# Kernel tuning notes

Hardware: AMD Instinct MI355X
Metric: run time of the kernel (lower is better)

## Reference

```python
import jax, jax.numpy as jnp
import numpy as np


def _log_kernel(ks, sigma):
    ax = np.arange(-(ks // 2), ks // 2 + 1, dtype=np.float64)
    xx, yy = np.meshgrid(ax, ax, indexing='ij')
    r2 = xx ** 2 + yy ** 2
    gaussian = np.exp(-r2 / (2 * sigma ** 2))
    laplacian = -1.0 / (np.pi * sigma ** 4) * (1.0 - r2 / (2 * sigma ** 2))
    k = laplacian * gaussian
    k = k / np.sum(np.abs(k))
    return jnp.asarray(k, jnp.float32)


def _hpf_kernel(ks):
    if ks == 3:
        k = np.array([[-1, -1, -1], [-1, 8, -1], [-1, -1, -1]], dtype=np.float32)
    else:  # 5
        k = -np.ones((5, 5), dtype=np.float32)
        k[2, 2] = 24.0
    return jnp.asarray(k)


def _lpf_kernel():
    k = np.array([[1, 2, 1], [2, 4, 2], [1, 2, 1]], dtype=np.float32) / 16.0
    return jnp.asarray(k)


def _gabor_kernel(angle, frequency=0.1, sigma_x=2.0, sigma_y=2.0):
    theta = np.radians(angle)
    x, y = np.meshgrid(np.linspace(-3, 3, 7), np.linspace(-3, 3, 7))
    x_t = x * np.cos(theta) + y * np.sin(theta)
    y_t = -x * np.sin(theta) + y * np.cos(theta)
    g = np.exp(-(x_t ** 2 / sigma_x ** 2 + y_t ** 2 / sigma_y ** 2) / 2.0) * np.cos(2 * np.pi * frequency * x_t)
    g = g / np.sum(np.abs(g))
    return jnp.asarray(g, jnp.float32)


def _dwconv(x, k2d, pad):
    # depthwise conv: same single-channel kernel applied to every channel
    C = x.shape[1]
    kern = jnp.broadcast_to(k2d[None, None], (C, 1) + k2d.shape)  # (C,1,kh,kw)
    return jax.lax.conv_general_dilated(
        x, kern, window_strides=(1, 1), padding=[(pad, pad), (pad, pad)],
        feature_group_count=C, dimension_numbers=('NCHW', 'OIHW', 'NCHW'))


def _squash(z):
    # (tanh(z*0.1)+1)/2
    return (jnp.tanh(z * 0.1) + 1.0) * 0.5


def setup_inputs() -> dict:
    key = jax.random.key(0)
    x = jax.random.normal(key, (16, 3, 512, 512), dtype=jnp.float32)
    return {"x": x, "use_gabor": 1}


def reference(x, use_gabor):
    # 'original'
    original = x
    # 'lpf'
    lpf = _dwconv(x, _lpf_kernel(), pad=1)
    # 'log': multi-scale LoG -> squash -> elementwise max over scales
    log3 = _dwconv(x, _log_kernel(3, 0.8), pad=1)
    log5 = _dwconv(x, _log_kernel(5, 1.0), pad=2)
    log7 = _dwconv(x, _log_kernel(7, 1.4), pad=3)
    log_out = jnp.maximum(jnp.maximum(_squash(log3), _squash(log5)), _squash(log7))
    # 'hpf'
    hpf3 = _dwconv(x, _hpf_kernel(3), pad=1)
    hpf5 = _dwconv(x, _hpf_kernel(5), pad=2)
    hpf_out = jnp.maximum(_squash(hpf3), _squash(hpf5))
    outs = (original, lpf, log_out, hpf_out)
    if use_gabor:
        gab = None
        for angle in (0, 45, 90, 135):
            r = jnp.tanh(_dwconv(x, _gabor_kernel(angle), pad=3) * 0.1)
            gab = r if gab is None else jnp.maximum(gab, r)
        outs = outs + (gab,)
    return outs
```

## Files before the change

### kernel.cpp

```cpp
#include <hip/hip_runtime.h>

#define IMG_H 512
#define IMG_W 512
#define TILE_W 64
#define TILE_H 16
#define LDSW 72
#define LDSH 22
#define NTHREADS 256


constexpr double PI_D = 3.141592653589793238462643383279502884;

constexpr double cexp(double x) {
  double term = 1.0, sum = 1.0;
  for (int n = 1; n < 48; ++n) { term *= x / n; sum += term; }
  return sum;
}
constexpr double ccos(double x) {
  double term = 1.0, sum = 1.0;
  for (int n = 1; n < 24; ++n) {
    term *= -x * x / ((2.0 * n - 1.0) * (2.0 * n));
    sum += term;
  }
  return sum;
}
constexpr double csin(double x) {
  double term = x, sum = x;
  for (int n = 1; n < 24; ++n) {
    term *= -x * x / ((2.0 * n) * (2.0 * n + 1.0));
    sum += term;
  }
  return sum;
}
constexpr double cabs_(double x) { return x < 0 ? -x : x; }

struct KTabs {
  float lpf[9];
  float log3[9];
  float log5[25];
  float log7[49];
  float hpf3[9];
  float hpf5[25];
  float gab[4][49];
};

constexpr void fill_log(int ks, double sigma, float* out) {
  double buf[49] = {};
  double s = 0.0;
  const int h = ks / 2;
  for (int i = 0; i < ks; ++i) {
    for (int j = 0; j < ks; ++j) {
      const double xi = (double)(i - h);
      const double yj = (double)(j - h);
      const double r2 = xi * xi + yj * yj;
      const double g = cexp(-r2 / (2.0 * sigma * sigma));
      const double lap = -1.0 / (PI_D * sigma * sigma * sigma * sigma) *
                         (1.0 - r2 / (2.0 * sigma * sigma));
      buf[i * ks + j] = lap * g;
      s += cabs_(lap * g);
    }
  }
  for (int k = 0; k < ks * ks; ++k) out[k] = (float)(buf[k] / s);
}

constexpr void fill_gabor(double ang_deg, float* out) {
  const double th = ang_deg * PI_D / 180.0;
  const double ct = ccos(th), st = csin(th);
  double buf[49] = {};
  double s = 0.0;
  for (int i = 0; i < 7; ++i) {
    for (int j = 0; j < 7; ++j) {
      const double xv = (double)(j - 3);
      const double yv = (double)(i - 3);
      const double xt = xv * ct + yv * st;
      const double yt = -xv * st + yv * ct;
      const double g = cexp(-(xt * xt / 4.0 + yt * yt / 4.0) / 2.0) *
                       ccos(2.0 * PI_D * 0.1 * xt);
      buf[i * 7 + j] = g;
      s += cabs_(g);
    }
  }
  for (int k = 0; k < 49; ++k) out[k] = (float)(buf[k] / s);
}

constexpr KTabs make_tabs() {
  KTabs t{};
  const double lv[9] = {1, 2, 1, 2, 4, 2, 1, 2, 1};
  for (int k = 0; k < 9; ++k) t.lpf[k] = (float)(lv[k] / 16.0);
  for (int k = 0; k < 9; ++k) t.hpf3[k] = -1.0f;
  t.hpf3[4] = 8.0f;
  for (int k = 0; k < 25; ++k) t.hpf5[k] = -1.0f;
  t.hpf5[12] = 24.0f;
  fill_log(3, 0.8, t.log3);
  fill_log(5, 1.0, t.log5);
  fill_log(7, 1.4, t.log7);
  fill_gabor(0.0, t.gab[0]);
  fill_gabor(45.0, t.gab[1]);
  fill_gabor(90.0, t.gab[2]);
  fill_gabor(135.0, t.gab[3]);
  return t;
}

constexpr KTabs KT = make_tabs();


__device__ __forceinline__ float fast_tanh(float x) {
  float e = __builtin_amdgcn_exp2f(x * 2.8853900817779268f);
  return 1.0f - 2.0f * __builtin_amdgcn_rcpf(e + 1.0f);
}
__device__ __forceinline__ float squash_from(float z) {
  return fmaf(fast_tanh(0.1f * z), 0.5f, 0.5f);
}

__global__ __launch_bounds__(NTHREADS)
void msif_kernel(const float* __restrict__ x, float* __restrict__ out,
                 int planes, int do_gab) {
  __shared__ float tile[LDSH * LDSW];
  const int tid = threadIdx.x;
  const int tx = tid & 15;
  const int ty = tid >> 4;
  const int x0 = blockIdx.x * TILE_W;
  const int y0 = blockIdx.y * TILE_H;
  const int plane = blockIdx.z;
  const float* __restrict__ in = x + (size_t)plane * (IMG_H * IMG_W);

  const int gx0 = x0 - 4;
  const int gy0 = y0 - 3;
  for (int k = tid; k < LDSH * (LDSW / 4); k += NTHREADS) {
    int r = k / (LDSW / 4);
    int cc = (k - r * (LDSW / 4)) * 4;
    int gy = gy0 + r;
    int gx = gx0 + cc;
    float4 v = make_float4(0.f, 0.f, 0.f, 0.f);
    if ((unsigned)gy < IMG_H) {
      const float* rowp = in + (size_t)gy * IMG_W;
      if (gx >= 0 && gx + 3 < IMG_W) {
        v = *(const float4*)(rowp + gx);
      } else {
        float t0 = 0.f, t1 = 0.f, t2 = 0.f, t3 = 0.f;
        if ((unsigned)(gx + 0) < IMG_W) t0 = rowp[gx + 0];
        if ((unsigned)(gx + 1) < IMG_W) t1 = rowp[gx + 1];
        if ((unsigned)(gx + 2) < IMG_W) t2 = rowp[gx + 2];
        if ((unsigned)(gx + 3) < IMG_W) t3 = rowp[gx + 3];
        v = make_float4(t0, t1, t2, t3);
      }
    }
    *(float4*)&tile[r * LDSW + cc] = v;
  }
  __syncthreads();

  float l7[4] = {}, l5[4] = {}, l3[4] = {};
  float h5[4] = {}, h3[4] = {}, lp[4] = {};
  float g0[4] = {}, g1[4] = {}, g2[4] = {}, g3[4] = {};

#pragma unroll
  for (int ir = 0; ir < 7; ++ir) {
    const float4* p = (const float4*)&tile[(ty + ir) * LDSW + 4 * tx];
    float4 w0 = p[0], w1 = p[1], w2 = p[2];
    float w[12] = {w0.x, w0.y, w0.z, w0.w, w1.x, w1.y, w1.z, w1.w,
                   w2.x, w2.y, w2.z, w2.w};

#pragma unroll
    for (int dx = 0; dx < 7; ++dx) {
      const float c7 = KT.log7[ir * 7 + dx];
      const float cg0 = KT.gab[0][ir * 7 + dx];
      const float cg1 = KT.gab[1][ir * 7 + dx];
      const float cg2 = KT.gab[2][ir * 7 + dx];
      const float cg3 = KT.gab[3][ir * 7 + dx];
#pragma unroll
      for (int c = 0; c < 4; ++c) {
        const float v = w[c + dx + 1];
        l7[c] = fmaf(v, c7, l7[c]);
        g0[c] = fmaf(v, cg0, g0[c]);
        g1[c] = fmaf(v, cg1, g1[c]);
        g2[c] = fmaf(v, cg2, g2[c]);
        g3[c] = fmaf(v, cg3, g3[c]);
      }
    }
    if (ir >= 1 && ir <= 5) {
      const int kr = ir - 1;
#pragma unroll
      for (int dx = 0; dx < 5; ++dx) {
        const float c5 = KT.log5[kr * 5 + dx];
        const float ch5 = KT.hpf5[kr * 5 + dx];
#pragma unroll
        for (int c = 0; c < 4; ++c) {
          const float v = w[c + dx + 2];
          l5[c] = fmaf(v, c5, l5[c]);
          h5[c] = fmaf(v, ch5, h5[c]);
        }
      }
    }
    if (ir >= 2 && ir <= 4) {
      const int kr = ir - 2;
#pragma unroll
      for (int dx = 0; dx < 3; ++dx) {
        const float cl = KT.lpf[kr * 3 + dx];
        const float c3 = KT.log3[kr * 3 + dx];
        const float ch3 = KT.hpf3[kr * 3 + dx];
#pragma unroll
        for (int c = 0; c < 4; ++c) {
          const float v = w[c + dx + 3];
          lp[c] = fmaf(v, cl, lp[c]);
          l3[c] = fmaf(v, c3, l3[c]);
          h3[c] = fmaf(v, ch3, h3[c]);
        }
      }
    }
  }

  const int X = x0 + 4 * tx;
  const int yo = y0 + ty;
  const size_t fs = (size_t)planes * (IMG_H * IMG_W);
  const size_t off = (size_t)plane * (IMG_H * IMG_W) + (size_t)yo * IMG_W + X;

  float4 orig = *(const float4*)&tile[(ty + 3) * LDSW + 4 * tx + 4];
  *(float4*)(out + off) = orig;

  float lo[4], ho[4], go[4];
#pragma unroll
  for (int c = 0; c < 4; ++c) {
    lo[c] = squash_from(fmaxf(fmaxf(l3[c], l5[c]), l7[c]));
    ho[c] = squash_from(fmaxf(h3[c], h5[c]));
    go[c] = fast_tanh(0.1f * fmaxf(fmaxf(g0[c], g1[c]), fmaxf(g2[c], g3[c])));
  }
  *(float4*)(out + fs + off) = make_float4(lp[0], lp[1], lp[2], lp[3]);
  *(float4*)(out + 2 * fs + off) = make_float4(lo[0], lo[1], lo[2], lo[3]);
  *(float4*)(out + 3 * fs + off) = make_float4(ho[0], ho[1], ho[2], ho[3]);
  if (do_gab)
    *(float4*)(out + 4 * fs + off) = make_float4(go[0], go[1], go[2], go[3]);
}

extern "C" void kernel_launch(void* const* d_in, const int* in_sizes, int n_in,
                              void* d_out, int out_size, void* d_ws, size_t ws_size,
                              hipStream_t stream) {
  const float* x = (const float*)d_in[0];
  float* out = (float*)d_out;
  const int plane_elems = IMG_H * IMG_W;
  const int planes = in_sizes[0] / plane_elems;
  const int do_gab = (out_size >= 5 * in_sizes[0]) ? 1 : 0;

  dim3 grid(IMG_W / TILE_W, IMG_H / TILE_H, planes);
  msif_kernel<<<grid, NTHREADS, 0, stream>>>(x, out, planes, do_gab);
}
```

Baseline: 317.3 us.

## Decompose LoG, Gabor and HPF stencils into separable vertical/horizontal passes via LDS

```diff
diff --git a/kernel.cpp b/kernel.cpp
--- a/kernel.cpp
+++ b/kernel.cpp
@@ -6,6 +6,8 @@
 #define TILE_H 16
 #define LDSW 72
 #define LDSH 22
+#define TCOLS 72
+#define TROWS 16
 #define NTHREADS 256
 
 
@@ -33,16 +35,6 @@
   return sum;
 }
 constexpr double cabs_(double x) { return x < 0 ? -x : x; }
-
-struct KTabs {
-  float lpf[9];
-  float log3[9];
-  float log5[25];
-  float log7[49];
-  float hpf3[9];
-  float hpf5[25];
-  float gab[4][49];
-};
 
 constexpr void fill_log(int ks, double sigma, float* out) {
   double buf[49] = {};
@@ -63,12 +55,33 @@
   for (int k = 0; k < ks * ks; ++k) out[k] = (float)(buf[k] / s);
 }
 
-constexpr void fill_gabor(double ang_deg, float* out) {
+constexpr void fill_log_sep(int ks, double sigma, float* va, float* g, float* wb) {
+  const int h = ks / 2;
+  double s = 0.0;
+  for (int i = 0; i < ks; ++i)
+    for (int j = 0; j < ks; ++j) {
+      const double xi = (double)(i - h), yj = (double)(j - h);
+      const double r2 = xi * xi + yj * yj;
+      const double gg = cexp(-r2 / (2.0 * sigma * sigma));
+      const double lap = -1.0 / (PI_D * sigma * sigma * sigma * sigma) *
+                         (1.0 - r2 / (2.0 * sigma * sigma));
+      s += cabs_(lap * gg);
+    }
+  const double c = 1.0 / (PI_D * sigma * sigma * sigma * sigma);
+  for (int i = 0; i < ks; ++i) {
+    const double d = (double)(i - h);
+    const double gi = cexp(-d * d / (2.0 * sigma * sigma));
+    g[i] = (float)gi;
+    va[i] = (float)((-c + c * d * d / (2.0 * sigma * sigma)) * gi / s);
+    wb[i] = (float)((c * d * d / (2.0 * sigma * sigma)) * gi / s);
+  }
+}
+
+constexpr double gabor_norm(double ang_deg) {
   const double th = ang_deg * PI_D / 180.0;
   const double ct = ccos(th), st = csin(th);
-  double buf[49] = {};
   double s = 0.0;
-  for (int i = 0; i < 7; ++i) {
+  for (int i = 0; i < 7; ++i)
     for (int j = 0; j < 7; ++j) {
       const double xv = (double)(j - 3);
       const double yv = (double)(i - 3);
@@ -76,32 +89,51 @@
       const double yt = -xv * st + yv * ct;
       const double g = cexp(-(xt * xt / 4.0 + yt * yt / 4.0) / 2.0) *
                        ccos(2.0 * PI_D * 0.1 * xt);
-      buf[i * 7 + j] = g;
       s += cabs_(g);
     }
-  }
-  for (int k = 0; k < 49; ++k) out[k] = (float)(buf[k] / s);
-}
-
-constexpr KTabs make_tabs() {
-  KTabs t{};
-  const double lv[9] = {1, 2, 1, 2, 4, 2, 1, 2, 1};
-  for (int k = 0; k < 9; ++k) t.lpf[k] = (float)(lv[k] / 16.0);
-  for (int k = 0; k < 9; ++k) t.hpf3[k] = -1.0f;
-  t.hpf3[4] = 8.0f;
-  for (int k = 0; k < 25; ++k) t.hpf5[k] = -1.0f;
-  t.hpf5[12] = 24.0f;
-  fill_log(3, 0.8, t.log3);
-  fill_log(5, 1.0, t.log5);
-  fill_log(7, 1.4, t.log7);
-  fill_gabor(0.0, t.gab[0]);
-  fill_gabor(45.0, t.gab[1]);
-  fill_gabor(90.0, t.gab[2]);
-  fill_gabor(135.0, t.gab[3]);
+  return s;
+}
+
+struct SepTabs {
+  float l5_va[5], l5_g[5], l5_wb[5];
+  float l7_va[7], l7_g[7], l7_wb[7];
+  float v_gb[7], v_gc0[7], v_gca[7], v_gsa[7];
+  float h_g0[7], h_g90[7], h_gc[7], h_gs[7];
+  float is45, is135;
+  float l3_m, l3_e, l3_s;
+};
+
+constexpr SepTabs make_sep() {
+  SepTabs t{};
+  fill_log_sep(5, 1.0, t.l5_va, t.l5_g, t.l5_wb);
+  fill_log_sep(7, 1.4, t.l7_va, t.l7_g, t.l7_wb);
+  const double s0 = gabor_norm(0.0), s90 = gabor_norm(90.0);
+  const double s45 = gabor_norm(45.0), s135 = gabor_norm(135.0);
+  const double th45 = 45.0 * PI_D / 180.0;
+  const double a45 = 2.0 * PI_D * 0.1 * ccos(th45);
+  const double b45 = 2.0 * PI_D * 0.1 * csin(th45);
+  const double w0 = 2.0 * PI_D * 0.1;
+  for (int k = 0; k < 7; ++k) {
+    const double d = (double)(k - 3);
+    const double gg = cexp(-d * d / 8.0);
+    t.v_gb[k]  = (float)gg;
+    t.v_gc0[k] = (float)(gg * ccos(w0 * d));
+    t.v_gca[k] = (float)(gg * ccos(b45 * d));
+    t.v_gsa[k] = (float)(gg * csin(b45 * d));
+    t.h_g0[k]  = (float)(gg * ccos(w0 * d) / s0);
+    t.h_g90[k] = (float)(gg / s90);
+    t.h_gc[k]  = (float)(gg * ccos(a45 * d));
+    t.h_gs[k]  = (float)(gg * csin(a45 * d));
+  }
+  t.is45 = (float)(1.0 / s45);
+  t.is135 = (float)(1.0 / s135);
+  float l3[9] = {};
+  fill_log(3, 0.8, l3);
+  t.l3_m = l3[4]; t.l3_e = l3[1]; t.l3_s = l3[0];
   return t;
 }
 
-constexpr KTabs KT = make_tabs();
+constexpr SepTabs ST = make_sep();
 
 
 __device__ __forceinline__ float fast_tanh(float x) {
@@ -111,11 +143,39 @@
 __device__ __forceinline__ float squash_from(float z) {
   return fmaf(fast_tanh(0.1f * z), 0.5f, 0.5f);
 }
+__device__ __forceinline__ float4 f4z() { return make_float4(0.f, 0.f, 0.f, 0.f); }
+__device__ __forceinline__ float4 f4add(float4 a, float4 b) {
+  return make_float4(a.x + b.x, a.y + b.y, a.z + b.z, a.w + b.w);
+}
+__device__ __forceinline__ float4 f4fma(float a, float4 b, float4 c) {
+  return make_float4(fmaf(a, b.x, c.x), fmaf(a, b.y, c.y),
+                     fmaf(a, b.z, c.z), fmaf(a, b.w, c.w));
+}
+__device__ __forceinline__ void loadw12(const float* p, float* w) {
+  const float4 a = *(const float4*)(p);
+  const float4 b = *(const float4*)(p + 4);
+  const float4 c = *(const float4*)(p + 8);
+  w[0] = a.x; w[1] = a.y; w[2] = a.z; w[3] = a.w;
+  w[4] = b.x; w[5] = b.y; w[6] = b.z; w[7] = b.w;
+  w[8] = c.x; w[9] = c.y; w[10] = c.z; w[11] = c.w;
+}
+
+#define T_B5  0
+#define T_L5A 1
+#define T_L5G 2
+#define T_L7A 3
+#define T_L7G 4
+#define T_GB  5
+#define T_GC0 6
+#define T_GCA 7
+#define T_GSA 8
 
 __global__ __launch_bounds__(NTHREADS)
 void msif_kernel(const float* __restrict__ x, float* __restrict__ out,
                  int planes, int do_gab) {
   __shared__ float tile[LDSH * LDSW];
+  __shared__ float T[9][TROWS * TCOLS];
+
   const int tid = threadIdx.x;
   const int tx = tid & 15;
   const int ty = tid >> 4;
@@ -149,80 +209,137 @@
   }
   __syncthreads();
 
-  float l7[4] = {}, l5[4] = {}, l3[4] = {};
-  float h5[4] = {}, h3[4] = {}, lp[4] = {};
-  float g0[4] = {}, g1[4] = {}, g2[4] = {}, g3[4] = {};
-
-#pragma unroll
-  for (int ir = 0; ir < 7; ++ir) {
-    const float4* p = (const float4*)&tile[(ty + ir) * LDSW + 4 * tx];
-    float4 w0 = p[0], w1 = p[1], w2 = p[2];
-    float w[12] = {w0.x, w0.y, w0.z, w0.w, w1.x, w1.y, w1.z, w1.w,
-                   w2.x, w2.y, w2.z, w2.w};
-
-#pragma unroll
-    for (int dx = 0; dx < 7; ++dx) {
-      const float c7 = KT.log7[ir * 7 + dx];
-      const float cg0 = KT.gab[0][ir * 7 + dx];
-      const float cg1 = KT.gab[1][ir * 7 + dx];
-      const float cg2 = KT.gab[2][ir * 7 + dx];
-      const float cg3 = KT.gab[3][ir * 7 + dx];
-#pragma unroll
-      for (int c = 0; c < 4; ++c) {
-        const float v = w[c + dx + 1];
-        l7[c] = fmaf(v, c7, l7[c]);
-        g0[c] = fmaf(v, cg0, g0[c]);
-        g1[c] = fmaf(v, cg1, g1[c]);
-        g2[c] = fmaf(v, cg2, g2[c]);
-        g3[c] = fmaf(v, cg3, g3[c]);
-      }
-    }
-    if (ir >= 1 && ir <= 5) {
-      const int kr = ir - 1;
-#pragma unroll
-      for (int dx = 0; dx < 5; ++dx) {
-        const float c5 = KT.log5[kr * 5 + dx];
-        const float ch5 = KT.hpf5[kr * 5 + dx];
-#pragma unroll
-        for (int c = 0; c < 4; ++c) {
-          const float v = w[c + dx + 2];
-          l5[c] = fmaf(v, c5, l5[c]);
-          h5[c] = fmaf(v, ch5, h5[c]);
-        }
-      }
-    }
-    if (ir >= 2 && ir <= 4) {
-      const int kr = ir - 2;
-#pragma unroll
-      for (int dx = 0; dx < 3; ++dx) {
-        const float cl = KT.lpf[kr * 3 + dx];
-        const float c3 = KT.log3[kr * 3 + dx];
-        const float ch3 = KT.hpf3[kr * 3 + dx];
-#pragma unroll
-        for (int c = 0; c < 4; ++c) {
-          const float v = w[c + dx + 3];
-          lp[c] = fmaf(v, cl, lp[c]);
-          l3[c] = fmaf(v, c3, l3[c]);
-          h3[c] = fmaf(v, ch3, h3[c]);
-        }
-      }
-    }
-  }
+  for (int k = tid; k < TROWS * (TCOLS / 4); k += NTHREADS) {
+    const int r = k / (TCOLS / 4);
+    const int c4 = (k - r * (TCOLS / 4)) * 4;
+    const float* base = &tile[r * LDSW + c4];
+    float4 wv[7];
+#pragma unroll
+    for (int i = 0; i < 7; ++i) wv[i] = *(const float4*)(base + i * LDSW);
+
+    float4 b5 = f4add(f4add(wv[1], wv[2]), f4add(f4add(wv[3], wv[4]), wv[5]));
+    float4 l5a = f4z(), l5g = f4z();
+#pragma unroll
+    for (int i = 0; i < 5; ++i) {
+      l5a = f4fma(ST.l5_va[i], wv[i + 1], l5a);
+      l5g = f4fma(ST.l5_g[i],  wv[i + 1], l5g);
+    }
+    float4 l7a = f4z(), l7g = f4z(), gb = f4z(), gc0 = f4z(), gca = f4z(), gsa = f4z();
+#pragma unroll
+    for (int i = 0; i < 7; ++i) {
+      l7a = f4fma(ST.l7_va[i], wv[i], l7a);
+      l7g = f4fma(ST.l7_g[i],  wv[i], l7g);
+      gb  = f4fma(ST.v_gb[i],  wv[i], gb);
+      gc0 = f4fma(ST.v_gc0[i], wv[i], gc0);
+      gca = f4fma(ST.v_gca[i], wv[i], gca);
+      gsa = f4fma(ST.v_gsa[i], wv[i], gsa);
+    }
+    const int o = r * TCOLS + c4;
+    *(float4*)&T[T_B5][o]  = b5;
+    *(float4*)&T[T_L5A][o] = l5a;
+    *(float4*)&T[T_L5G][o] = l5g;
+    *(float4*)&T[T_L7A][o] = l7a;
+    *(float4*)&T[T_L7G][o] = l7g;
+    *(float4*)&T[T_GB][o]  = gb;
+    *(float4*)&T[T_GC0][o] = gc0;
+    *(float4*)&T[T_GCA][o] = gca;
+    *(float4*)&T[T_GSA][o] = gsa;
+  }
+  __syncthreads();
+
+  const int toff = ty * TCOLS + 4 * tx;
+  float w[12];
+  float l7[4] = {}, l5[4] = {}, g0[4] = {}, g90[4] = {}, Pa[4] = {}, Qa[4] = {};
+  float box[4];
+
+  loadw12(&T[T_L7A][toff], w);
+#pragma unroll
+  for (int dx = 0; dx < 7; ++dx) {
+    const float cc = ST.l7_g[dx];
+#pragma unroll
+    for (int c = 0; c < 4; ++c) l7[c] = fmaf(w[c + dx + 1], cc, l7[c]);
+  }
+  loadw12(&T[T_L7G][toff], w);
+#pragma unroll
+  for (int dx = 0; dx < 7; ++dx) {
+    const float cc = ST.l7_wb[dx];
+#pragma unroll
+    for (int c = 0; c < 4; ++c) l7[c] = fmaf(w[c + dx + 1], cc, l7[c]);
+  }
+  loadw12(&T[T_L5A][toff], w);
+#pragma unroll
+  for (int dx = 0; dx < 5; ++dx) {
+    const float cc = ST.l5_g[dx];
+#pragma unroll
+    for (int c = 0; c < 4; ++c) l5[c] = fmaf(w[c + dx + 2], cc, l5[c]);
+  }
+  loadw12(&T[T_L5G][toff], w);
+#pragma unroll
+  for (int dx = 0; dx < 5; ++dx) {
+    const float cc = ST.l5_wb[dx];
+#pragma unroll
+    for (int c = 0; c < 4; ++c) l5[c] = fmaf(w[c + dx + 2], cc, l5[c]);
+  }
+  loadw12(&T[T_B5][toff], w);
+#pragma unroll
+  for (int c = 0; c < 4; ++c)
+    box[c] = ((w[c + 2] + w[c + 3]) + (w[c + 4] + w[c + 5])) + w[c + 6];
+  loadw12(&T[T_GB][toff], w);
+#pragma unroll
+  for (int dx = 0; dx < 7; ++dx) {
+    const float cc = ST.h_g0[dx];
+#pragma unroll
+    for (int c = 0; c < 4; ++c) g0[c] = fmaf(w[c + dx + 1], cc, g0[c]);
+  }
+  loadw12(&T[T_GC0][toff], w);
+#pragma unroll
+  for (int dx = 0; dx < 7; ++dx) {
+    const float cc = ST.h_g90[dx];
+#pragma unroll
+    for (int c = 0; c < 4; ++c) g90[c] = fmaf(w[c + dx + 1], cc, g90[c]);
+  }
+  loadw12(&T[T_GCA][toff], w);
+#pragma unroll
+  for (int dx = 0; dx < 7; ++dx) {
+    const float cc = ST.h_gc[dx];
+#pragma unroll
+    for (int c = 0; c < 4; ++c) Pa[c] = fmaf(w[c + dx + 1], cc, Pa[c]);
+  }
+  loadw12(&T[T_GSA][toff], w);
+#pragma unroll
+  for (int dx = 0; dx < 7; ++dx) {
+    const float cc = ST.h_gs[dx];
+#pragma unroll
+    for (int c = 0; c < 4; ++c) Qa[c] = fmaf(w[c + dx + 1], cc, Qa[c]);
+  }
+
+  float tr[12], mr[12], br[12];
+  loadw12(&tile[(ty + 2) * LDSW + 4 * tx], tr);
+  loadw12(&tile[(ty + 3) * LDSW + 4 * tx], mr);
+  loadw12(&tile[(ty + 4) * LDSW + 4 * tx], br);
 
   const int X = x0 + 4 * tx;
   const int yo = y0 + ty;
   const size_t fs = (size_t)planes * (IMG_H * IMG_W);
   const size_t off = (size_t)plane * (IMG_H * IMG_W) + (size_t)yo * IMG_W + X;
 
-  float4 orig = *(const float4*)&tile[(ty + 3) * LDSW + 4 * tx + 4];
-  *(float4*)(out + off) = orig;
-
-  float lo[4], ho[4], go[4];
+  *(float4*)(out + off) = make_float4(mr[4], mr[5], mr[6], mr[7]);
+
+  float lp[4], lo[4], ho[4], go[4];
 #pragma unroll
   for (int c = 0; c < 4; ++c) {
-    lo[c] = squash_from(fmaxf(fmaxf(l3[c], l5[c]), l7[c]));
-    ho[c] = squash_from(fmaxf(h3[c], h5[c]));
-    go[c] = fast_tanh(0.1f * fmaxf(fmaxf(g0[c], g1[c]), fmaxf(g2[c], g3[c])));
+    const float mC = mr[c + 4];
+    const float e  = (tr[c + 4] + br[c + 4]) + (mr[c + 3] + mr[c + 5]);
+    const float sC = (tr[c + 3] + tr[c + 5]) + (br[c + 3] + br[c + 5]);
+    lp[c] = fmaf(0.25f, mC, fmaf(0.125f, e, 0.0625f * sC));
+    const float l3v = fmaf(ST.l3_m, mC, fmaf(ST.l3_e, e, ST.l3_s * sC));
+    const float h3v = fmaf(8.f, mC, -(e + sC));
+    const float h5v = fmaf(25.f, mC, -box[c]);
+    lo[c] = squash_from(fmaxf(fmaxf(l3v, l5[c]), l7[c]));
+    ho[c] = squash_from(fmaxf(h3v, h5v));
+    const float o45  = (Pa[c] - Qa[c]) * ST.is45;
+    const float o135 = (Pa[c] + Qa[c]) * ST.is135;
+    go[c] = fast_tanh(0.1f * fmaxf(fmaxf(g0[c], g90[c]), fmaxf(o45, o135)));
   }
   *(float4*)(out + fs + off) = make_float4(lp[0], lp[1], lp[2], lp[3]);
   *(float4*)(out + 2 * fs + off) = make_float4(lo[0], lo[1], lo[2], lo[3]);
```

Result: slower. 328.5 us (+3.5%).

## Process multiple tiles per block with double-buffered LDS prefetch and nontemporal stores

Applied to the files above, without the earlier changes.

```diff
diff --git a/kernel.cpp b/kernel.cpp
--- a/kernel.cpp
+++ b/kernel.cpp
@@ -4,9 +4,14 @@
 #define IMG_W 512
 #define TILE_W 64
 #define TILE_H 16
+#define TILES_X (IMG_W / TILE_W)
+#define TILES_Y (IMG_H / TILE_H)
+#define TILES_PER_PLANE (TILES_X * TILES_Y)
 #define LDSW 72
 #define LDSH 22
+#define NSLOTS (LDSH * (LDSW / 4))
 #define NTHREADS 256
+#define TPB 12
 
 
 constexpr double PI_D = 3.141592653589793238462643383279502884;
@@ -104,6 +109,8 @@
 constexpr KTabs KT = make_tabs();
 
 
+typedef float f4v __attribute__((ext_vector_type(4)));
+
 __device__ __forceinline__ float fast_tanh(float x) {
   float e = __builtin_amdgcn_exp2f(x * 2.8853900817779268f);
   return 1.0f - 2.0f * __builtin_amdgcn_rcpf(e + 1.0f);
@@ -112,123 +119,175 @@
   return fmaf(fast_tanh(0.1f * z), 0.5f, 0.5f);
 }
 
+__device__ __forceinline__ void store_nt(float* p, float a, float b, float c,
+                                         float d) {
+  f4v v = {a, b, c, d};
+  __builtin_nontemporal_store(v, (f4v*)p);
+}
+
+__device__ __forceinline__ float4 guarded_load(const float* __restrict__ in,
+                                               int gy, int gx) {
+  float4 v = make_float4(0.f, 0.f, 0.f, 0.f);
+  if ((unsigned)gy < IMG_H) {
+    const float* rowp = in + (size_t)gy * IMG_W;
+    if (gx >= 0 && gx + 3 < IMG_W) {
+      v = *(const float4*)(rowp + gx);
+    } else {
+      if ((unsigned)(gx + 0) < IMG_W) v.x = rowp[gx + 0];
+      if ((unsigned)(gx + 1) < IMG_W) v.y = rowp[gx + 1];
+      if ((unsigned)(gx + 2) < IMG_W) v.z = rowp[gx + 2];
+      if ((unsigned)(gx + 3) < IMG_W) v.w = rowp[gx + 3];
+    }
+  }
+  return v;
+}
+
+__device__ __forceinline__ void tile_decode(int t, int& x0, int& y0, int& pl) {
+  pl = t >> 8;
+  const int rem = t & 255;
+  y0 = (rem >> 3) * TILE_H;
+  x0 = (rem & 7) * TILE_W;
+}
+
+
 __global__ __launch_bounds__(NTHREADS)
 void msif_kernel(const float* __restrict__ x, float* __restrict__ out,
-                 int planes, int do_gab) {
-  __shared__ float tile[LDSH * LDSW];
+                 int planes, int do_gab, int tiles_total) {
+  __shared__ float lds[2][LDSH * LDSW];
+
   const int tid = threadIdx.x;
   const int tx = tid & 15;
   const int ty = tid >> 4;
-  const int x0 = blockIdx.x * TILE_W;
-  const int y0 = blockIdx.y * TILE_H;
-  const int plane = blockIdx.z;
-  const float* __restrict__ in = x + (size_t)plane * (IMG_H * IMG_W);
-
-  const int gx0 = x0 - 4;
-  const int gy0 = y0 - 3;
-  for (int k = tid; k < LDSH * (LDSW / 4); k += NTHREADS) {
-    int r = k / (LDSW / 4);
-    int cc = (k - r * (LDSW / 4)) * 4;
-    int gy = gy0 + r;
-    int gx = gx0 + cc;
-    float4 v = make_float4(0.f, 0.f, 0.f, 0.f);
-    if ((unsigned)gy < IMG_H) {
-      const float* rowp = in + (size_t)gy * IMG_W;
-      if (gx >= 0 && gx + 3 < IMG_W) {
-        v = *(const float4*)(rowp + gx);
-      } else {
-        float t0 = 0.f, t1 = 0.f, t2 = 0.f, t3 = 0.f;
-        if ((unsigned)(gx + 0) < IMG_W) t0 = rowp[gx + 0];
-        if ((unsigned)(gx + 1) < IMG_W) t1 = rowp[gx + 1];
-        if ((unsigned)(gx + 2) < IMG_W) t2 = rowp[gx + 2];
-        if ((unsigned)(gx + 3) < IMG_W) t3 = rowp[gx + 3];
-        v = make_float4(t0, t1, t2, t3);
-      }
-    }
-    *(float4*)&tile[r * LDSW + cc] = v;
+  const int rA = tid / (LDSW / 4);
+  const int cA = (tid % (LDSW / 4)) * 4;
+  const int slotB = tid + NTHREADS;
+  const bool hasB = slotB < NSLOTS;
+  const int rB = slotB / (LDSW / 4);
+  const int cB = (slotB % (LDSW / 4)) * 4;
+
+  const int t0 = blockIdx.x * TPB;
+  if (t0 >= tiles_total) return;
+
+  const size_t fs = (size_t)planes * (IMG_H * IMG_W);
+
+  {
+    int x0, y0, pl;
+    tile_decode(t0, x0, y0, pl);
+    const float* in = x + (size_t)pl * (IMG_H * IMG_W);
+    const float4 va = guarded_load(in, y0 - 3 + rA, x0 - 4 + cA);
+    float4 vb = make_float4(0.f, 0.f, 0.f, 0.f);
+    if (hasB) vb = guarded_load(in, y0 - 3 + rB, x0 - 4 + cB);
+    *(float4*)&lds[0][rA * LDSW + cA] = va;
+    if (hasB) *(float4*)&lds[0][rB * LDSW + cB] = vb;
   }
   __syncthreads();
 
-  float l7[4] = {}, l5[4] = {}, l3[4] = {};
-  float h5[4] = {}, h3[4] = {}, lp[4] = {};
-  float g0[4] = {}, g1[4] = {}, g2[4] = {}, g3[4] = {};
-
-#pragma unroll
-  for (int ir = 0; ir < 7; ++ir) {
-    const float4* p = (const float4*)&tile[(ty + ir) * LDSW + 4 * tx];
-    float4 w0 = p[0], w1 = p[1], w2 = p[2];
-    float w[12] = {w0.x, w0.y, w0.z, w0.w, w1.x, w1.y, w1.z, w1.w,
-                   w2.x, w2.y, w2.z, w2.w};
-
-#pragma unroll
-    for (int dx = 0; dx < 7; ++dx) {
-      const float c7 = KT.log7[ir * 7 + dx];
-      const float cg0 = KT.gab[0][ir * 7 + dx];
-      const float cg1 = KT.gab[1][ir * 7 + dx];
-      const float cg2 = KT.gab[2][ir * 7 + dx];
-      const float cg3 = KT.gab[3][ir * 7 + dx];
-#pragma unroll
-      for (int c = 0; c < 4; ++c) {
-        const float v = w[c + dx + 1];
-        l7[c] = fmaf(v, c7, l7[c]);
-        g0[c] = fmaf(v, cg0, g0[c]);
-        g1[c] = fmaf(v, cg1, g1[c]);
-        g2[c] = fmaf(v, cg2, g2[c]);
-        g3[c] = fmaf(v, cg3, g3[c]);
-      }
-    }
-    if (ir >= 1 && ir <= 5) {
-      const int kr = ir - 1;
-#pragma unroll
-      for (int dx = 0; dx < 5; ++dx) {
-        const float c5 = KT.log5[kr * 5 + dx];
-        const float ch5 = KT.hpf5[kr * 5 + dx];
+  int cur = 0;
+  for (int i = 0; i < TPB; ++i) {
+    const int t = t0 + i;
+    if (t >= tiles_total) break;
+    int x0, y0, pl;
+    tile_decode(t, x0, y0, pl);
+    const bool havenext = (i + 1 < TPB) && (t + 1 < tiles_total);
+
+    float4 va = make_float4(0.f, 0.f, 0.f, 0.f);
+    float4 vb = make_float4(0.f, 0.f, 0.f, 0.f);
+    if (havenext) {
+      int nx0, ny0, npl;
+      tile_decode(t + 1, nx0, ny0, npl);
+      const float* nin = x + (size_t)npl * (IMG_H * IMG_W);
+      va = guarded_load(nin, ny0 - 3 + rA, nx0 - 4 + cA);
+      if (hasB) vb = guarded_load(nin, ny0 - 3 + rB, nx0 - 4 + cB);
+    }
+
+    const float* __restrict__ tl = lds[cur];
+
+    float l7[4] = {}, l5[4] = {}, l3[4] = {};
+    float h5[4] = {}, h3[4] = {}, lp[4] = {};
+    float g0[4] = {}, g1[4] = {}, g2[4] = {}, g3[4] = {};
+
+#pragma unroll
+    for (int ir = 0; ir < 7; ++ir) {
+      const float4* p = (const float4*)&tl[(ty + ir) * LDSW + 4 * tx];
+      float4 w0 = p[0], w1 = p[1], w2 = p[2];
+      float w[12] = {w0.x, w0.y, w0.z, w0.w, w1.x, w1.y, w1.z, w1.w,
+                     w2.x, w2.y, w2.z, w2.w};
+
+#pragma unroll
+      for (int dx = 0; dx < 7; ++dx) {
+        const float c7 = KT.log7[ir * 7 + dx];
+        const float cg0 = KT.gab[0][ir * 7 + dx];
+        const float cg1 = KT.gab[1][ir * 7 + dx];
+        const float cg2 = KT.gab[2][ir * 7 + dx];
+        const float cg3 = KT.gab[3][ir * 7 + dx];
 #pragma unroll
         for (int c = 0; c < 4; ++c) {
-          const float v = w[c + dx + 2];
-          l5[c] = fmaf(v, c5, l5[c]);
-          h5[c] = fmaf(v, ch5, h5[c]);
+          const float v = w[c + dx + 1];
+          l7[c] = fmaf(v, c7, l7[c]);
+          g0[c] = fmaf(v, cg0, g0[c]);
+          g1[c] = fmaf(v, cg1, g1[c]);
+          g2[c] = fmaf(v, cg2, g2[c]);
+          g3[c] = fmaf(v, cg3, g3[c]);
         }
       }
-    }
-    if (ir >= 2 && ir <= 4) {
-      const int kr = ir - 2;
-#pragma unroll
-      for (int dx = 0; dx < 3; ++dx) {
-        const float cl = KT.lpf[kr * 3 + dx];
-        const float c3 = KT.log3[kr * 3 + dx];
-        const float ch3 = KT.hpf3[kr * 3 + dx];
-#pragma unroll
-        for (int c = 0; c < 4; ++c) {
-          const float v = w[c + dx + 3];
-          lp[c] = fmaf(v, cl, lp[c]);
-          l3[c] = fmaf(v, c3, l3[c]);
-          h3[c] = fmaf(v, ch3, h3[c]);
+      if (ir >= 1 && ir <= 5) {
+        const int kr = ir - 1;
+#pragma unroll
+        for (int dx = 0; dx < 5; ++dx) {
+          const float c5 = KT.log5[kr * 5 + dx];
+          const float ch5 = KT.hpf5[kr * 5 + dx];
+#pragma unroll
+          for (int c = 0; c < 4; ++c) {
+            const float v = w[c + dx + 2];
+            l5[c] = fmaf(v, c5, l5[c]);
+            h5[c] = fmaf(v, ch5, h5[c]);
+          }
         }
       }
-    }
-  }
-
-  const int X = x0 + 4 * tx;
-  const int yo = y0 + ty;
-  const size_t fs = (size_t)planes * (IMG_H * IMG_W);
-  const size_t off = (size_t)plane * (IMG_H * IMG_W) + (size_t)yo * IMG_W + X;
-
-  float4 orig = *(const float4*)&tile[(ty + 3) * LDSW + 4 * tx + 4];
-  *(float4*)(out + off) = orig;
-
-  float lo[4], ho[4], go[4];
-#pragma unroll
-  for (int c = 0; c < 4; ++c) {
-    lo[c] = squash_from(fmaxf(fmaxf(l3[c], l5[c]), l7[c]));
-    ho[c] = squash_from(fmaxf(h3[c], h5[c]));
-    go[c] = fast_tanh(0.1f * fmaxf(fmaxf(g0[c], g1[c]), fmaxf(g2[c], g3[c])));
-  }
-  *(float4*)(out + fs + off) = make_float4(lp[0], lp[1], lp[2], lp[3]);
-  *(float4*)(out + 2 * fs + off) = make_float4(lo[0], lo[1], lo[2], lo[3]);
-  *(float4*)(out + 3 * fs + off) = make_float4(ho[0], ho[1], ho[2], ho[3]);
-  if (do_gab)
-    *(float4*)(out + 4 * fs + off) = make_float4(go[0], go[1], go[2], go[3]);
+      if (ir >= 2 && ir <= 4) {
+        const int kr = ir - 2;
+#pragma unroll
+        for (int dx = 0; dx < 3; ++dx) {
+          const float cl = KT.lpf[kr * 3 + dx];
+          const float c3 = KT.log3[kr * 3 + dx];
+          const float ch3 = KT.hpf3[kr * 3 + dx];
+#pragma unroll
+          for (int c = 0; c < 4; ++c) {
+            const float v = w[c + dx + 3];
+            lp[c] = fmaf(v, cl, lp[c]);
+            l3[c] = fmaf(v, c3, l3[c]);
+            h3[c] = fmaf(v, ch3, h3[c]);
+          }
+        }
+      }
+    }
+
+    const int X = x0 + 4 * tx;
+    const int yo = y0 + ty;
+    const size_t off = (size_t)pl * (IMG_H * IMG_W) + (size_t)yo * IMG_W + X;
+
+    const float4 orig = *(const float4*)&tl[(ty + 3) * LDSW + 4 * tx + 4];
+    store_nt(out + off, orig.x, orig.y, orig.z, orig.w);
+
+    float lo[4], ho[4], go[4];
+#pragma unroll
+    for (int c = 0; c < 4; ++c) {
+      lo[c] = squash_from(fmaxf(fmaxf(l3[c], l5[c]), l7[c]));
+      ho[c] = squash_from(fmaxf(h3[c], h5[c]));
+      go[c] = fast_tanh(0.1f * fmaxf(fmaxf(g0[c], g1[c]), fmaxf(g2[c], g3[c])));
+    }
+    store_nt(out + fs + off, lp[0], lp[1], lp[2], lp[3]);
+    store_nt(out + 2 * fs + off, lo[0], lo[1], lo[2], lo[3]);
+    store_nt(out + 3 * fs + off, ho[0], ho[1], ho[2], ho[3]);
+    if (do_gab) store_nt(out + 4 * fs + off, go[0], go[1], go[2], go[3]);
+
+    if (havenext) {
+      *(float4*)&lds[cur ^ 1][rA * LDSW + cA] = va;
+      if (hasB) *(float4*)&lds[cur ^ 1][rB * LDSW + cB] = vb;
+      __syncthreads();
+      cur ^= 1;
+    }
+  }
 }
 
 extern "C" void kernel_launch(void* const* d_in, const int* in_sizes, int n_in,
@@ -239,7 +298,9 @@
   const int plane_elems = IMG_H * IMG_W;
   const int planes = in_sizes[0] / plane_elems;
   const int do_gab = (out_size >= 5 * in_sizes[0]) ? 1 : 0;
-
-  dim3 grid(IMG_W / TILE_W, IMG_H / TILE_H, planes);
-  msif_kernel<<<grid, NTHREADS, 0, stream>>>(x, out, planes, do_gab);
-}
+  const int tiles_total = planes * TILES_PER_PLANE;
+  const int nblocks = (tiles_total + TPB - 1) / TPB;
+
+  msif_kernel<<<dim3(nblocks), NTHREADS, 0, stream>>>(x, out, planes, do_gab,
+                                                      tiles_total);
+}
```

Result: slower. 345.1 us (+8.7%).

## Tile full-width row bands per block to eliminate horizontal halo reloads

Applied to the files above, without the earlier changes.

```diff
diff --git a/kernel.cpp b/kernel.cpp
--- a/kernel.cpp
+++ b/kernel.cpp
@@ -2,10 +2,11 @@
 
 #define IMG_H 512
 #define IMG_W 512
-#define TILE_W 64
 #define TILE_H 16
-#define LDSW 72
+#define BANDS (IMG_H / TILE_H)
+#define LDSW 520
 #define LDSH 22
+#define ROWSLOTS (LDSW / 4)
 #define NTHREADS 256
 
 
@@ -112,123 +113,126 @@
   return fmaf(fast_tanh(0.1f * z), 0.5f, 0.5f);
 }
 
+
 __global__ __launch_bounds__(NTHREADS)
 void msif_kernel(const float* __restrict__ x, float* __restrict__ out,
                  int planes, int do_gab) {
   __shared__ float tile[LDSH * LDSW];
+
   const int tid = threadIdx.x;
-  const int tx = tid & 15;
-  const int ty = tid >> 4;
-  const int x0 = blockIdx.x * TILE_W;
-  const int y0 = blockIdx.y * TILE_H;
-  const int plane = blockIdx.z;
-  const float* __restrict__ in = x + (size_t)plane * (IMG_H * IMG_W);
-
-  const int gx0 = x0 - 4;
+  const int lane = tid & 63;
+  const int wv = tid >> 6;
+  const int b = blockIdx.x;
+  const int pl = b >> 5;
+  const int band = b & 31;
+  const int y0 = band * TILE_H;
+  const float* __restrict__ in = x + (size_t)pl * (IMG_H * IMG_W);
+
   const int gy0 = y0 - 3;
-  for (int k = tid; k < LDSH * (LDSW / 4); k += NTHREADS) {
-    int r = k / (LDSW / 4);
-    int cc = (k - r * (LDSW / 4)) * 4;
-    int gy = gy0 + r;
-    int gx = gx0 + cc;
+  for (int sl = tid; sl < LDSH * ROWSLOTS; sl += NTHREADS) {
+    const int r = sl / ROWSLOTS;
+    const int c = sl - r * ROWSLOTS;
+    const int gy = gy0 + r;
     float4 v = make_float4(0.f, 0.f, 0.f, 0.f);
-    if ((unsigned)gy < IMG_H) {
-      const float* rowp = in + (size_t)gy * IMG_W;
-      if (gx >= 0 && gx + 3 < IMG_W) {
-        v = *(const float4*)(rowp + gx);
-      } else {
-        float t0 = 0.f, t1 = 0.f, t2 = 0.f, t3 = 0.f;
-        if ((unsigned)(gx + 0) < IMG_W) t0 = rowp[gx + 0];
-        if ((unsigned)(gx + 1) < IMG_W) t1 = rowp[gx + 1];
-        if ((unsigned)(gx + 2) < IMG_W) t2 = rowp[gx + 2];
-        if ((unsigned)(gx + 3) < IMG_W) t3 = rowp[gx + 3];
-        v = make_float4(t0, t1, t2, t3);
-      }
-    }
-    *(float4*)&tile[r * LDSW + cc] = v;
+    if ((unsigned)gy < IMG_H && (unsigned)(c - 1) < 128u)
+      v = *(const float4*)(in + (size_t)gy * IMG_W + (size_t)(c - 1) * 4);
+    *(float4*)&tile[r * LDSW + 4 * c] = v;
   }
   __syncthreads();
 
-  float l7[4] = {}, l5[4] = {}, l3[4] = {};
-  float h5[4] = {}, h3[4] = {}, lp[4] = {};
-  float g0[4] = {}, g1[4] = {}, g2[4] = {}, g3[4] = {};
-
-#pragma unroll
-  for (int ir = 0; ir < 7; ++ir) {
-    const float4* p = (const float4*)&tile[(ty + ir) * LDSW + 4 * tx];
-    float4 w0 = p[0], w1 = p[1], w2 = p[2];
-    float w[12] = {w0.x, w0.y, w0.z, w0.w, w1.x, w1.y, w1.z, w1.w,
-                   w2.x, w2.y, w2.z, w2.w};
-
-#pragma unroll
-    for (int dx = 0; dx < 7; ++dx) {
-      const float c7 = KT.log7[ir * 7 + dx];
-      const float cg0 = KT.gab[0][ir * 7 + dx];
-      const float cg1 = KT.gab[1][ir * 7 + dx];
-      const float cg2 = KT.gab[2][ir * 7 + dx];
-      const float cg3 = KT.gab[3][ir * 7 + dx];
-#pragma unroll
-      for (int c = 0; c < 4; ++c) {
-        const float v = w[c + dx + 1];
-        l7[c] = fmaf(v, c7, l7[c]);
-        g0[c] = fmaf(v, cg0, g0[c]);
-        g1[c] = fmaf(v, cg1, g1[c]);
-        g2[c] = fmaf(v, cg2, g2[c]);
-        g3[c] = fmaf(v, cg3, g3[c]);
-      }
-    }
-    if (ir >= 1 && ir <= 5) {
-      const int kr = ir - 1;
-#pragma unroll
-      for (int dx = 0; dx < 5; ++dx) {
-        const float c5 = KT.log5[kr * 5 + dx];
-        const float ch5 = KT.hpf5[kr * 5 + dx];
-#pragma unroll
-        for (int c = 0; c < 4; ++c) {
-          const float v = w[c + dx + 2];
-          l5[c] = fmaf(v, c5, l5[c]);
-          h5[c] = fmaf(v, ch5, h5[c]);
+  const size_t fs = (size_t)planes * (IMG_H * IMG_W);
+
+#pragma unroll 1
+  for (int it = 0; it < 4; ++it) {
+    const int yl = wv + 4 * it;
+#pragma unroll 1
+    for (int s = 0; s < 2; ++s) {
+      const int colbase = 256 * s + 4 * lane;
+
+      float l7[4] = {}, l5[4] = {}, l3[4] = {};
+      float h5[4] = {}, h3[4] = {}, lp[4] = {};
+      float g0[4] = {}, g1[4] = {}, g2[4] = {}, g3[4] = {};
+      float4 orig = make_float4(0.f, 0.f, 0.f, 0.f);
+
+#pragma unroll
+      for (int ir = 0; ir < 7; ++ir) {
+        const float4* p =
+            (const float4*)&tile[(yl + ir) * LDSW + colbase];
+        float4 w0 = p[0], w1 = p[1], w2 = p[2];
+        float w[12] = {w0.x, w0.y, w0.z, w0.w, w1.x, w1.y, w1.z, w1.w,
+                       w2.x, w2.y, w2.z, w2.w};
+        if (ir == 3) orig = make_float4(w[4], w[5], w[6], w[7]);
+
+#pragma unroll
+        for (int dx = 0; dx < 7; ++dx) {
+          const float c7 = KT.log7[ir * 7 + dx];
+          const float cg0 = KT.gab[0][ir * 7 + dx];
+          const float cg1 = KT.gab[1][ir * 7 + dx];
+          const float cg2 = KT.gab[2][ir * 7 + dx];
+          const float cg3 = KT.gab[3][ir * 7 + dx];
+#pragma unroll
+          for (int c = 0; c < 4; ++c) {
+            const float v = w[c + dx + 1];
+            l7[c] = fmaf(v, c7, l7[c]);
+            g0[c] = fmaf(v, cg0, g0[c]);
+            g1[c] = fmaf(v, cg1, g1[c]);
+            g2[c] = fmaf(v, cg2, g2[c]);
+            g3[c] = fmaf(v, cg3, g3[c]);
+          }
+        }
+        if (ir >= 1 && ir <= 5) {
+          const int kr = ir - 1;
+#pragma unroll
+          for (int dx = 0; dx < 5; ++dx) {
+            const float c5 = KT.log5[kr * 5 + dx];
+            const float ch5 = KT.hpf5[kr * 5 + dx];
+#pragma unroll
+            for (int c = 0; c < 4; ++c) {
+              const float v = w[c + dx + 2];
+              l5[c] = fmaf(v, c5, l5[c]);
+              h5[c] = fmaf(v, ch5, h5[c]);
+            }
+          }
+        }
+        if (ir >= 2 && ir <= 4) {
+          const int kr = ir - 2;
+#pragma unroll
+          for (int dx = 0; dx < 3; ++dx) {
+            const float cl = KT.lpf[kr * 3 + dx];
+            const float c3 = KT.log3[kr * 3 + dx];
+            const float ch3 = KT.hpf3[kr * 3 + dx];
+#pragma unroll
+            for (int c = 0; c < 4; ++c) {
+              const float v = w[c + dx + 3];
+              lp[c] = fmaf(v, cl, lp[c]);
+              l3[c] = fmaf(v, c3, l3[c]);
+              h3[c] = fmaf(v, ch3, h3[c]);
+            }
+          }
         }
       }
+
+      const int yo = y0 + yl;
+      const size_t off =
+          (size_t)pl * (IMG_H * IMG_W) + (size_t)yo * IMG_W + colbase;
+
+      *(float4*)(out + off) = orig;
+
+      float lo[4], ho[4], go[4];
+#pragma unroll
+      for (int c = 0; c < 4; ++c) {
+        lo[c] = squash_from(fmaxf(fmaxf(l3[c], l5[c]), l7[c]));
+        ho[c] = squash_from(fmaxf(h3[c], h5[c]));
+        go[c] =
+            fast_tanh(0.1f * fmaxf(fmaxf(g0[c], g1[c]), fmaxf(g2[c], g3[c])));
+      }
+      *(float4*)(out + fs + off) = make_float4(lp[0], lp[1], lp[2], lp[3]);
+      *(float4*)(out + 2 * fs + off) = make_float4(lo[0], lo[1], lo[2], lo[3]);
+      *(float4*)(out + 3 * fs + off) = make_float4(ho[0], ho[1], ho[2], ho[3]);
+      if (do_gab)
+        *(float4*)(out + 4 * fs + off) = make_float4(go[0], go[1], go[2], go[3]);
     }
-    if (ir >= 2 && ir <= 4) {
-      const int kr = ir - 2;
-#pragma unroll
-      for (int dx = 0; dx < 3; ++dx) {
-        const float cl = KT.lpf[kr * 3 + dx];
-        const float c3 = KT.log3[kr * 3 + dx];
-        const float ch3 = KT.hpf3[kr * 3 + dx];
-#pragma unroll
-        for (int c = 0; c < 4; ++c) {
-          const float v = w[c + dx + 3];
-          lp[c] = fmaf(v, cl, lp[c]);
-          l3[c] = fmaf(v, c3, l3[c]);
-          h3[c] = fmaf(v, ch3, h3[c]);
-        }
-      }
-    }
-  }
-
-  const int X = x0 + 4 * tx;
-  const int yo = y0 + ty;
-  const size_t fs = (size_t)planes * (IMG_H * IMG_W);
-  const size_t off = (size_t)plane * (IMG_H * IMG_W) + (size_t)yo * IMG_W + X;
-
-  float4 orig = *(const float4*)&tile[(ty + 3) * LDSW + 4 * tx + 4];
-  *(float4*)(out + off) = orig;
-
-  float lo[4], ho[4], go[4];
-#pragma unroll
-  for (int c = 0; c < 4; ++c) {
-    lo[c] = squash_from(fmaxf(fmaxf(l3[c], l5[c]), l7[c]));
-    ho[c] = squash_from(fmaxf(h3[c], h5[c]));
-    go[c] = fast_tanh(0.1f * fmaxf(fmaxf(g0[c], g1[c]), fmaxf(g2[c], g3[c])));
-  }
-  *(float4*)(out + fs + off) = make_float4(lp[0], lp[1], lp[2], lp[3]);
-  *(float4*)(out + 2 * fs + off) = make_float4(lo[0], lo[1], lo[2], lo[3]);
-  *(float4*)(out + 3 * fs + off) = make_float4(ho[0], ho[1], ho[2], ho[3]);
-  if (do_gab)
-    *(float4*)(out + 4 * fs + off) = make_float4(go[0], go[1], go[2], go[3]);
+  }
 }
 
 extern "C" void kernel_launch(void* const* d_in, const int* in_sizes, int n_in,
@@ -240,6 +244,6 @@
   const int planes = in_sizes[0] / plane_elems;
   const int do_gab = (out_size >= 5 * in_sizes[0]) ? 1 : 0;
 
-  dim3 grid(IMG_W / TILE_W, IMG_H / TILE_H, planes);
-  msif_kernel<<<grid, NTHREADS, 0, stream>>>(x, out, planes, do_gab);
-}
+  msif_kernel<<<dim3(planes * BANDS), NTHREADS, 0, stream>>>(x, out, planes,
+                                                             do_gab);
+}
```

New measurement: 334.0 us. 5.3% more time.
